# Performance work log

Hardware: AMD Instinct MI355X
Metric: run time of the kernel (lower is better)

The kernel has to match this reference:

```python
import jax, jax.numpy as jnp
import numpy as np

B, C, N, H = 4, 256, 2048, 8
D = C // H
EPS = 1e-5

def setup_inputs() -> dict:
    key = jax.random.key(0)
    ks = jax.random.split(key, 5)
    return {
        "x": jax.random.normal(ks[0], (B, C, N), jnp.float32),
        "w_qkv": jax.random.normal(ks[1], (3 * C, C), jnp.float32) * (C ** -0.5),
        "b_qkv": jax.random.normal(ks[2], (3 * C,), jnp.float32) * 0.02,
        "w_proj": jax.random.normal(ks[3], (C, C), jnp.float32) * (C ** -0.5),
        "b_proj": jax.random.normal(ks[4], (C,), jnp.float32) * 0.02,
        "ln_g": jnp.ones((C,), jnp.float32),
        "ln_b": jnp.zeros((C,), jnp.float32),
    }

def reference(x, w_qkv, b_qkv, w_proj, b_proj, ln_g, ln_b):
    # QKV 1x1 conv == per-point linear: [B,3C,N]
    qkv = jnp.einsum('oc,bcn->bon', w_qkv, x) + b_qkv[:, None]
    # [B,3,H,D,N] -> q,k,v each [B,H,N,D]
    qkv = qkv.reshape(B, 3, H, D, N).transpose(1, 0, 2, 4, 3)
    q, k, v = qkv[0], qkv[1], qkv[2]
    scale = D ** -0.5
    attn = jax.nn.softmax(jnp.einsum('bhnd,bhmd->bhnm', q, k) * scale, axis=-1)
    # dropout is identity in eval mode
    out = jnp.einsum('bhnm,bhmd->bhnd', attn, v)  # [B,H,N,D]
    out = out.transpose(0, 1, 3, 2).reshape(B, C, N)
    out = jnp.einsum('oc,bcn->bon', w_proj, out) + b_proj[:, None]
    out = out + x
    # LayerNorm over channel dim
    o = out.transpose(0, 2, 1)  # [B,N,C]
    mu = jnp.mean(o, axis=-1, keepdims=True)
    var = jnp.mean((o - mu) ** 2, axis=-1, keepdims=True)
    o = (o - mu) * jax.lax.rsqrt(var + EPS) * ln_g + ln_b
    return o.transpose(0, 2, 1)  # [B,C,N]
```

## Files before the change

### kernel.cpp

```cpp
#include <hip/hip_runtime.h>
#include <hip/hip_bf16.h>

#define Bx 4
#define Cx 256
#define Nx 2048
#define Hx 8
#define Dx 32

typedef __attribute__((ext_vector_type(8))) short bf16x8;
typedef __attribute__((ext_vector_type(4))) float f32x4;

#define QSCALE 0.25503494f

static __device__ __forceinline__ unsigned short f2bf(float f) {
    unsigned int u = __float_as_uint(f);
    u += 0x7fffu + ((u >> 16) & 1u);
    return (unsigned short)(u >> 16);
}
static __device__ __forceinline__ float bf2f(unsigned short u) {
    return __uint_as_float(((unsigned int)u) << 16);
}
static __device__ __forceinline__ float fexp2(float x) {
    float r;
    asm("v_exp_f32 %0, %1" : "=v"(r) : "v"(x));
    return r;
}
static __device__ __forceinline__ float frcp(float x) {
    float r;
    asm("v_rcp_f32 %0, %1" : "=v"(r) : "v"(x));
    return r;
}

__global__ __launch_bounds__(256) void convert_kernel(
    const float* __restrict__ x, const float* __restrict__ w_qkv,
    const float* __restrict__ w_proj,
    unsigned short* __restrict__ Xt, unsigned short* __restrict__ Wqkvb,
    unsigned short* __restrict__ Wpb)
{
    const int bx = blockIdx.x, t = threadIdx.x;
    if (bx < 512) {
        const int nb = (bx & 31) * 256 + t;
        const int b = nb >> 11, n = nb & 2047;
        const int c0 = (bx >> 5) * 16;
        const float* xb = x + (size_t)b * Cx * Nx + n;
        unsigned short* dst = Xt + ((size_t)b * Nx + n) * Cx;
        #pragma unroll
        for (int c8 = 0; c8 < 16; c8 += 8) {
            float f[8];
            #pragma unroll
            for (int j = 0; j < 8; ++j) f[j] = xb[(size_t)(c0 + c8 + j) * Nx];
            uint4 pk;
            pk.x = (unsigned)f2bf(f[0]) | ((unsigned)f2bf(f[1]) << 16);
            pk.y = (unsigned)f2bf(f[2]) | ((unsigned)f2bf(f[3]) << 16);
            pk.z = (unsigned)f2bf(f[4]) | ((unsigned)f2bf(f[5]) << 16);
            pk.w = (unsigned)f2bf(f[6]) | ((unsigned)f2bf(f[7]) << 16);
            *(uint4*)&dst[c0 + c8] = pk;
        }
    } else {
        const int flat = (bx - 512) * 2048 + t * 8;
        #pragma unroll
        for (int hh = 0; hh < 8; hh += 4) {
            const int f0 = flat + hh;
            if (f0 < 768 * 256) {
                const float sc = (f0 < 65536) ? QSCALE : 1.0f;
                const float4 f = *(const float4*)&w_qkv[f0];
                ushort4 o;
                o.x = f2bf(f.x * sc); o.y = f2bf(f.y * sc);
                o.z = f2bf(f.z * sc); o.w = f2bf(f.w * sc);
                *(ushort4*)&Wqkvb[f0] = o;
            } else {
                const int f2v = f0 - 768 * 256;
                const float4 f = *(const float4*)&w_proj[f2v];
                ushort4 o;
                o.x = f2bf(f.x); o.y = f2bf(f.y);
                o.z = f2bf(f.z); o.w = f2bf(f.w);
                *(ushort4*)&Wpb[f2v] = o;
            }
        }
    }
}

__global__ __launch_bounds__(256) void qkv_kernel(
    const unsigned short* __restrict__ Wb, const unsigned short* __restrict__ Xt,
    const float* __restrict__ bias,
    unsigned short* __restrict__ Qb, unsigned short* __restrict__ Kb,
    unsigned short* __restrict__ Vb)
{
    const int t = threadIdx.x;
    const int wv = t >> 6, l = t & 63;
    const int g = l >> 4, c = l & 15;

    const int lin = blockIdx.x + 12 * (blockIdx.y + 16 * blockIdx.z);
    const int xcd = lin & 7, s = lin >> 3;
    const int xb = s % 12;
    const int yz = (s / 12) * 8 + xcd;
    const int yb = yz & 15, b = yz >> 4;

    const int o0 = xb * 64 + (wv >> 1) * 32;
    const int n0 = yb * 128 + (wv & 1) * 64;
    const int region = xb >> 2;

    const unsigned short* XtB = Xt + (size_t)b * Nx * Cx;

    if (region < 2) {
        f32x4 acc[2][4];
        #pragma unroll
        for (int i = 0; i < 2; ++i)
            #pragma unroll
            for (int j = 0; j < 4; ++j) acc[i][j] = (f32x4){0.f, 0.f, 0.f, 0.f};

        for (int cc = 0; cc < Cx; cc += 32) {
            bf16x8 wf[2], xf[4];
            #pragma unroll
            for (int ti = 0; ti < 2; ++ti)
                wf[ti] = *(const bf16x8*)&Wb[(size_t)(o0 + ti * 16 + c) * Cx + cc + g * 8];
            #pragma unroll
            for (int tj = 0; tj < 4; ++tj)
                xf[tj] = *(const bf16x8*)&XtB[(size_t)(n0 + tj * 16 + c) * Cx + cc + g * 8];
            #pragma unroll
            for (int ti = 0; ti < 2; ++ti)
                #pragma unroll
                for (int tj = 0; tj < 4; ++tj)
                    acc[ti][tj] = __builtin_amdgcn_mfma_f32_16x16x32_bf16(
                        wf[ti], xf[tj], acc[ti][tj], 0, 0, 0);
        }

        unsigned short* dst = (region == 0) ? Qb : Kb;
        #pragma unroll
        for (int ti = 0; ti < 2; ++ti) {
            const int o = o0 + ti * 16 + g * 4;
            float4 bv = *(const float4*)&bias[o];
            if (region == 0) { bv.x *= QSCALE; bv.y *= QSCALE; bv.z *= QSCALE; bv.w *= QSCALE; }
            const int d0 = o & 31, bh = b * 8 + ((o >> 5) & 7);
            unsigned short* dp = dst + (size_t)bh * Nx * Dx + d0;
            #pragma unroll
            for (int tj = 0; tj < 4; ++tj) {
                const int n = n0 + tj * 16 + c;
                ushort4 w4;
                w4.x = f2bf(acc[ti][tj][0] + bv.x);
                w4.y = f2bf(acc[ti][tj][1] + bv.y);
                w4.z = f2bf(acc[ti][tj][2] + bv.z);
                w4.w = f2bf(acc[ti][tj][3] + bv.w);
                *(ushort4*)&dp[(size_t)n * Dx] = w4;
            }
        }
    } else {
        f32x4 acc[4][2];
        #pragma unroll
        for (int i = 0; i < 4; ++i)
            #pragma unroll
            for (int j = 0; j < 2; ++j) acc[i][j] = (f32x4){0.f, 0.f, 0.f, 0.f};

        for (int cc = 0; cc < Cx; cc += 32) {
            bf16x8 wf[2], xf[4];
            #pragma unroll
            for (int ot = 0; ot < 2; ++ot)
                wf[ot] = *(const bf16x8*)&Wb[(size_t)(o0 + ot * 16 + c) * Cx + cc + g * 8];
            #pragma unroll
            for (int nt = 0; nt < 4; ++nt)
                xf[nt] = *(const bf16x8*)&XtB[(size_t)(n0 + nt * 16 + c) * Cx + cc + g * 8];
            #pragma unroll
            for (int nt = 0; nt < 4; ++nt)
                #pragma unroll
                for (int ot = 0; ot < 2; ++ot)
                    acc[nt][ot] = __builtin_amdgcn_mfma_f32_16x16x32_bf16(
                        xf[nt], wf[ot], acc[nt][ot], 0, 0, 0);
        }

        #pragma unroll
        for (int ot = 0; ot < 2; ++ot) {
            const int o = o0 + ot * 16 + c;
            const float bv = bias[o];
            const int oV = o - 512, d = oV & 31, bh = b * 8 + (oV >> 5);
            unsigned short* dp = Vb + ((size_t)bh * Dx + d) * Nx;
            #pragma unroll
            for (int nt = 0; nt < 4; ++nt) {
                const int n = n0 + nt * 16 + g * 4;
                ushort4 w4;
                w4.x = f2bf(acc[nt][ot][0] + bv);
                w4.y = f2bf(acc[nt][ot][1] + bv);
                w4.z = f2bf(acc[nt][ot][2] + bv);
                w4.w = f2bf(acc[nt][ot][3] + bv);
                *(ushort4*)&dp[n] = w4;
            }
        }
    }
}

__global__ __launch_bounds__(256, 4) void attn_kernel(
    const unsigned short* __restrict__ Qb, const unsigned short* __restrict__ Kb,
    const unsigned short* __restrict__ Vb, unsigned short* __restrict__ Opart,
    float2* __restrict__ ML)
{
    const int t  = threadIdx.x;
    const int wv = t >> 6, l = t & 63;
    const int g  = l >> 4, c = l & 15;

    const int lin = blockIdx.x + 16 * blockIdx.y + 512 * blockIdx.z;
    const int xcd = lin & 7, s = lin >> 3;
    const int bh = ((s & 3) << 3) | xcd;
    const int qt_ = (s >> 2) & 15;
    const int z  = s >> 6;
    const int q0 = qt_ * 128 + wv * 32;

    const unsigned short* Qp = Qb + (size_t)bh * Nx * Dx;
    const unsigned short* Kp = Kb + (size_t)bh * Nx * Dx;
    const unsigned short* Vp = Vb + (size_t)bh * Dx * Nx;

    bf16x8 qf[2];
    #pragma unroll
    for (int qt = 0; qt < 2; ++qt)
        qf[qt] = *(const bf16x8*)&Qp[(size_t)(q0 + qt * 16 + c) * Dx + g * 8];

    union { unsigned int u[4]; bf16x8 v; } onesf;
    onesf.u[0] = onesf.u[1] = onesf.u[2] = onesf.u[3] = 0x3F803F80u;

    f32x4 oacc[2][2];
    f32x4 lacc[2];
    #pragma unroll
    for (int i = 0; i < 2; ++i) {
        lacc[i] = (f32x4){0.f, 0.f, 0.f, 0.f};
        #pragma unroll
        for (int j = 0; j < 2; ++j)
            oacc[i][j] = (f32x4){0.f, 0.f, 0.f, 0.f};
    }
    float m_i[2] = {-3.0e38f, -3.0e38f};
    const f32x4 zacc = (f32x4){0.f, 0.f, 0.f, 0.f};

    const int rowperm = (c >> 2) * 8 + (c & 3);

    const int kv_beg = z * (Nx / 2), kv_end = kv_beg + (Nx / 2);
    for (int kv0 = kv_beg; kv0 < kv_end; kv0 += 64) {
        bf16x8 kf[4];
        kf[0] = *(const bf16x8*)&Kp[(size_t)(kv0 + rowperm +  0) * Dx + g * 8];
        kf[1] = *(const bf16x8*)&Kp[(size_t)(kv0 + rowperm +  4) * Dx + g * 8];
        kf[2] = *(const bf16x8*)&Kp[(size_t)(kv0 + rowperm + 32) * Dx + g * 8];
        kf[3] = *(const bf16x8*)&Kp[(size_t)(kv0 + rowperm + 36) * Dx + g * 8];
        bf16x8 vf[2][2];
        #pragma unroll
        for (int dt = 0; dt < 2; ++dt)
            #pragma unroll
            for (int kc = 0; kc < 2; ++kc)
                vf[dt][kc] = *(const bf16x8*)
                    &Vp[(size_t)(dt * 16 + c) * Nx + kv0 + kc * 32 + g * 8];

        #pragma unroll
        for (int qt = 0; qt < 2; ++qt) {
            f32x4 sacc[4];
            #pragma unroll
            for (int ct = 0; ct < 4; ++ct)
                sacc[ct] = __builtin_amdgcn_mfma_f32_16x16x32_bf16(
                    kf[ct], qf[qt], zacc, 0, 0, 0);

            float tm[4];
            #pragma unroll
            for (int ct = 0; ct < 4; ++ct)
                tm[ct] = fmaxf(fmaxf(fmaxf(sacc[ct][0], sacc[ct][1]),
                                     sacc[ct][2]), sacc[ct][3]);
            const float mxl = fmaxf(fmaxf(fmaxf(tm[0], tm[1]), tm[2]), tm[3]);

            if (__any(mxl > m_i[qt] + 8.f)) {
                float mx = fmaxf(mxl, __shfl_xor(mxl, 16, 64));
                mx = fmaxf(mx, __shfl_xor(mx, 32, 64));
                const float mnew = fmaxf(m_i[qt], mx);
                const float aq = fexp2(m_i[qt] - mnew);
                m_i[qt] = mnew;
                #pragma unroll
                for (int dt = 0; dt < 2; ++dt)
                    #pragma unroll
                    for (int r = 0; r < 4; ++r) oacc[dt][qt][r] *= aq;
                #pragma unroll
                for (int r = 0; r < 4; ++r) lacc[qt][r] *= aq;
            }
            const float mcur = m_i[qt];
            unsigned int pw[4][2];
            #pragma unroll
            for (int ct = 0; ct < 4; ++ct) {
                float p[4];
                #pragma unroll
                for (int r = 0; r < 4; ++r) p[r] = fexp2(sacc[ct][r] - mcur);
                pw[ct][0] = (__float_as_uint(p[0]) >> 16) |
                            (__float_as_uint(p[1]) & 0xffff0000u);
                pw[ct][1] = (__float_as_uint(p[2]) >> 16) |
                            (__float_as_uint(p[3]) & 0xffff0000u);
            }

            #pragma unroll
            for (int kc = 0; kc < 2; ++kc) {
                union { unsigned int u[4]; bf16x8 v; } bw;
                bw.u[0] = pw[kc * 2 + 0][0];
                bw.u[1] = pw[kc * 2 + 0][1];
                bw.u[2] = pw[kc * 2 + 1][0];
                bw.u[3] = pw[kc * 2 + 1][1];
                oacc[0][qt] = __builtin_amdgcn_mfma_f32_16x16x32_bf16(
                    vf[0][kc], bw.v, oacc[0][qt], 0, 0, 0);
                oacc[1][qt] = __builtin_amdgcn_mfma_f32_16x16x32_bf16(
                    vf[1][kc], bw.v, oacc[1][qt], 0, 0, 0);
                lacc[qt] = __builtin_amdgcn_mfma_f32_16x16x32_bf16(
                    onesf.v, bw.v, lacc[qt], 0, 0, 0);
            }
        }
    }

    unsigned short* Op = Opart + ((size_t)(z * 32 + bh)) * Nx * Dx;
    float2* Mlp = ML + (size_t)(z * 32 + bh) * Nx;
    #pragma unroll
    for (int qt = 0; qt < 2; ++qt) {
        const int q = q0 + qt * 16 + c;
        if (g == 0) Mlp[q] = make_float2(m_i[qt], lacc[qt][0]);
        #pragma unroll
        for (int dt = 0; dt < 2; ++dt) {
            ushort4 w4;
            w4.x = f2bf(oacc[dt][qt][0]);
            w4.y = f2bf(oacc[dt][qt][1]);
            w4.z = f2bf(oacc[dt][qt][2]);
            w4.w = f2bf(oacc[dt][qt][3]);
            *(ushort4*)&Op[(size_t)q * Dx + dt * 16 + g * 4] = w4;
        }
    }
}

__global__ __launch_bounds__(256) void proj_ln_kernel(
    const unsigned short* __restrict__ Opart, const float2* __restrict__ ML,
    const unsigned short* __restrict__ Wpb,
    const float* __restrict__ bp, const float* __restrict__ x,
    const float* __restrict__ lng, const float* __restrict__ lnb,
    float* __restrict__ out)
{
    __shared__ float red[4][16];
    __shared__ float redq[4][16];
    __shared__ float mv[2][16];

    const int t  = threadIdx.x;
    const int wv = t >> 6, l = t & 63;
    const int lg = l >> 4, lc = l & 15;
    const int n0 = blockIdx.x * 16;
    const int b  = blockIdx.y;
    const int o0 = wv * 64;
    const int n  = n0 + lc;

    f32x4 acc[4];
    #pragma unroll
    for (int i = 0; i < 4; ++i) acc[i] = (f32x4){0.f, 0.f, 0.f, 0.f};

    for (int cc = 0; cc < Cx; cc += 32) {
        const int h = cc >> 5;
        const int bh = b * 8 + h;
        const float2 e0 = ML[(size_t)bh * Nx + n];
        const float2 e1 = ML[(size_t)(32 + bh) * Nx + n];
        const float M  = fmaxf(e0.x, e1.x);
        const float a0 = fexp2(e0.x - M), a1 = fexp2(e1.x - M);
        const float inv = frcp(e0.y * a0 + e1.y * a1);
        const float w0 = a0 * inv, w1 = a1 * inv;
        const size_t obase = ((size_t)bh * Nx + n) * Dx + lg * 8;
        const uint4 u0 = *(const uint4*)&Opart[obase];
        const uint4 u1 = *(const uint4*)&Opart[(size_t)65536 * Dx + obase];
        const unsigned int u0w[4] = {u0.x, u0.y, u0.z, u0.w};
        const unsigned int u1w[4] = {u1.x, u1.y, u1.z, u1.w};
        union { unsigned int u[4]; bf16x8 v; } af;
        #pragma unroll
        for (int wi = 0; wi < 4; ++wi) {
            const float lo = bf2f((unsigned short)(u0w[wi] & 0xffffu)) * w0 +
                             bf2f((unsigned short)(u1w[wi] & 0xffffu)) * w1;
            const float hi = bf2f((unsigned short)(u0w[wi] >> 16)) * w0 +
                             bf2f((unsigned short)(u1w[wi] >> 16)) * w1;
            af.u[wi] = (unsigned int)f2bf(lo) | ((unsigned int)f2bf(hi) << 16);
        }
        #pragma unroll
        for (int ti = 0; ti < 4; ++ti) {
            const bf16x8 wf = *(const bf16x8*)
                &Wpb[(size_t)(o0 + ti * 16 + lc) * Cx + cc + lg * 8];
            acc[ti] = __builtin_amdgcn_mfma_f32_16x16x32_bf16(wf, af.v, acc[ti], 0, 0, 0);
        }
    }

    #pragma unroll
    for (int ti = 0; ti < 4; ++ti) {
        const int o = o0 + ti * 16 + lg * 4;
        const float4 bv = *(const float4*)&bp[o];
        const float* xp = &x[((size_t)b * Cx + o) * Nx + n];
        acc[ti][0] += bv.x + xp[0];
        acc[ti][1] += bv.y + xp[Nx];
        acc[ti][2] += bv.z + xp[2 * Nx];
        acc[ti][3] += bv.w + xp[3 * Nx];
    }

    float s_ = 0.f, q_ = 0.f;
    #pragma unroll
    for (int ti = 0; ti < 4; ++ti)
        #pragma unroll
        for (int r = 0; r < 4; ++r) {
            const float v = acc[ti][r];
            s_ += v; q_ += v * v;
        }
    s_ += __shfl_xor(s_, 16, 64);
    s_ += __shfl_xor(s_, 32, 64);
    q_ += __shfl_xor(q_, 16, 64);
    q_ += __shfl_xor(q_, 32, 64);
    if (lg == 0) { red[wv][lc] = s_; redq[wv][lc] = q_; }
    __syncthreads();
    if (t < 16) {
        const float S = red[0][t] + red[1][t] + red[2][t] + red[3][t];
        const float Q = redq[0][t] + redq[1][t] + redq[2][t] + redq[3][t];
        const float mu  = S * (1.f / 256.f);
        const float var = Q * (1.f / 256.f) - mu * mu;
        mv[0][t] = mu;
        mv[1][t] = rsqrtf(var + 1e-5f);
    }
    __syncthreads();

    const float mu_ = mv[0][lc], rs_ = mv[1][lc];
    #pragma unroll
    for (int ti = 0; ti < 4; ++ti) {
        const int o = o0 + ti * 16 + lg * 4;
        const float4 g4 = *(const float4*)&lng[o];
        const float4 b4 = *(const float4*)&lnb[o];
        const float gr[4] = {g4.x, g4.y, g4.z, g4.w};
        const float br[4] = {b4.x, b4.y, b4.z, b4.w};
        float* op = &out[((size_t)b * Cx + o) * Nx + n];
        #pragma unroll
        for (int r = 0; r < 4; ++r)
            op[(size_t)r * Nx] = (acc[ti][r] - mu_) * rs_ * gr[r] + br[r];
    }
}

extern "C" void kernel_launch(void* const* d_in, const int* in_sizes, int n_in,
                              void* d_out, int out_size, void* d_ws, size_t ws_size,
                              hipStream_t stream) {
    (void)in_sizes; (void)n_in; (void)out_size; (void)ws_size;
    const float* x      = (const float*)d_in[0];
    const float* w_qkv  = (const float*)d_in[1];
    const float* b_qkv  = (const float*)d_in[2];
    const float* w_proj = (const float*)d_in[3];
    const float* b_proj = (const float*)d_in[4];
    const float* ln_g   = (const float*)d_in[5];
    const float* ln_b   = (const float*)d_in[6];
    float* out = (float*)d_out;

    char* wsb = (char*)d_ws;
    unsigned short* Xt    = (unsigned short*)(wsb);
    unsigned short* Wqkvb = (unsigned short*)(wsb + (size_t)4 * 1024 * 1024);
    unsigned short* Wpb   = (unsigned short*)(wsb + (size_t)4 * 1024 * 1024 + 393216);
    unsigned short* Qb    = (unsigned short*)(wsb + (size_t)5 * 1024 * 1024);
    unsigned short* Kb    = (unsigned short*)(wsb + (size_t)9 * 1024 * 1024);
    unsigned short* Vb    = (unsigned short*)(wsb + (size_t)13 * 1024 * 1024);
    unsigned short* Opart = (unsigned short*)(wsb + (size_t)21 * 1024 * 1024);
    float2*         ML    = (float2*)(wsb + (size_t)29 * 1024 * 1024);

    convert_kernel<<<dim3(640), 256, 0, stream>>>(x, w_qkv, w_proj, Xt, Wqkvb, Wpb);
    qkv_kernel<<<dim3(12, 16, 4), 256, 0, stream>>>(Wqkvb, Xt, b_qkv, Qb, Kb, Vb);
    attn_kernel<<<dim3(16, 32, 2), 256, 0, stream>>>(Qb, Kb, Vb, Opart, ML);
    proj_ln_kernel<<<dim3(128, 4), 256, 0, stream>>>(Opart, ML, Wpb, b_proj, x,
                                                     ln_g, ln_b, out);
}
```

Baseline: 155.9 us.

## Split attention KV range four ways and double-buffer K/V register loads

The attention kernel now splits each head's KV sequence into four chunks instead of two, doubling the grid to add parallelism. Each block's KV loop is fully unrolled with A/B register buffers, so the next tile's K/V loads are issued before the current tile is computed. The projection/LayerNorm kernel now merges four partial outputs and their max/sum statistics instead of two. The workspace is rearranged so the larger partial-output buffer reuses the space of the already-consumed transposed input. The cost is more partial-output traffic, extra merge work and higher register pressure from the prefetch buffers.

```diff
diff --git a/kernel.cpp b/kernel.cpp
--- a/kernel.cpp
+++ b/kernel.cpp
@@ -187,6 +187,80 @@
     }
 }
 
+static __device__ __forceinline__ void attn_tile(
+    const bf16x8* kf, const bf16x8* vf, const bf16x8* qf, bf16x8 onesv,
+    f32x4 (&oacc)[2][2], f32x4 (&lacc)[2], float (&m_i)[2])
+{
+    const f32x4 zacc = (f32x4){0.f, 0.f, 0.f, 0.f};
+    #pragma unroll
+    for (int qt = 0; qt < 2; ++qt) {
+        f32x4 sacc[4];
+        #pragma unroll
+        for (int ct = 0; ct < 4; ++ct)
+            sacc[ct] = __builtin_amdgcn_mfma_f32_16x16x32_bf16(
+                kf[ct], qf[qt], zacc, 0, 0, 0);
+
+        float tm[4];
+        #pragma unroll
+        for (int ct = 0; ct < 4; ++ct)
+            tm[ct] = fmaxf(fmaxf(fmaxf(sacc[ct][0], sacc[ct][1]),
+                                 sacc[ct][2]), sacc[ct][3]);
+        const float mxl = fmaxf(fmaxf(fmaxf(tm[0], tm[1]), tm[2]), tm[3]);
+
+        if (__any(mxl > m_i[qt] + 8.f)) {
+            float mx = fmaxf(mxl, __shfl_xor(mxl, 16, 64));
+            mx = fmaxf(mx, __shfl_xor(mx, 32, 64));
+            const float mnew = fmaxf(m_i[qt], mx);
+            const float aq = fexp2(m_i[qt] - mnew);
+            m_i[qt] = mnew;
+            #pragma unroll
+            for (int dt = 0; dt < 2; ++dt)
+                #pragma unroll
+                for (int r = 0; r < 4; ++r) oacc[dt][qt][r] *= aq;
+            #pragma unroll
+            for (int r = 0; r < 4; ++r) lacc[qt][r] *= aq;
+        }
+        const float mcur = m_i[qt];
+        unsigned int pw[4][2];
+        #pragma unroll
+        for (int ct = 0; ct < 4; ++ct) {
+            float p[4];
+            #pragma unroll
+            for (int r = 0; r < 4; ++r) p[r] = fexp2(sacc[ct][r] - mcur);
+            pw[ct][0] = (__float_as_uint(p[0]) >> 16) |
+                        (__float_as_uint(p[1]) & 0xffff0000u);
+            pw[ct][1] = (__float_as_uint(p[2]) >> 16) |
+                        (__float_as_uint(p[3]) & 0xffff0000u);
+        }
+
+        #pragma unroll
+        for (int kc = 0; kc < 2; ++kc) {
+            union { unsigned int u[4]; bf16x8 v; } bw;
+            bw.u[0] = pw[kc * 2 + 0][0];
+            bw.u[1] = pw[kc * 2 + 0][1];
+            bw.u[2] = pw[kc * 2 + 1][0];
+            bw.u[3] = pw[kc * 2 + 1][1];
+            oacc[0][qt] = __builtin_amdgcn_mfma_f32_16x16x32_bf16(
+                vf[0 * 2 + kc], bw.v, oacc[0][qt], 0, 0, 0);
+            oacc[1][qt] = __builtin_amdgcn_mfma_f32_16x16x32_bf16(
+                vf[1 * 2 + kc], bw.v, oacc[1][qt], 0, 0, 0);
+            lacc[qt] = __builtin_amdgcn_mfma_f32_16x16x32_bf16(
+                onesv, bw.v, lacc[qt], 0, 0, 0);
+        }
+    }
+}
+
+#define LOADT(KF, VF, KV) do {                                                  \
+    KF[0] = *(const bf16x8*)&Kp[(size_t)((KV) + rowperm +  0) * Dx + g * 8];    \
+    KF[1] = *(const bf16x8*)&Kp[(size_t)((KV) + rowperm +  4) * Dx + g * 8];    \
+    KF[2] = *(const bf16x8*)&Kp[(size_t)((KV) + rowperm + 32) * Dx + g * 8];    \
+    KF[3] = *(const bf16x8*)&Kp[(size_t)((KV) + rowperm + 36) * Dx + g * 8];    \
+    VF[0] = *(const bf16x8*)&Vp[(size_t)(c)      * Nx + (KV)      + g * 8];     \
+    VF[1] = *(const bf16x8*)&Vp[(size_t)(c)      * Nx + (KV) + 32 + g * 8];     \
+    VF[2] = *(const bf16x8*)&Vp[(size_t)(16 + c) * Nx + (KV)      + g * 8];     \
+    VF[3] = *(const bf16x8*)&Vp[(size_t)(16 + c) * Nx + (KV) + 32 + g * 8];     \
+} while (0)
+
 __global__ __launch_bounds__(256, 4) void attn_kernel(
     const unsigned short* __restrict__ Qb, const unsigned short* __restrict__ Kb,
     const unsigned short* __restrict__ Vb, unsigned short* __restrict__ Opart,
@@ -225,81 +299,23 @@
             oacc[i][j] = (f32x4){0.f, 0.f, 0.f, 0.f};
     }
     float m_i[2] = {-3.0e38f, -3.0e38f};
-    const f32x4 zacc = (f32x4){0.f, 0.f, 0.f, 0.f};
 
     const int rowperm = (c >> 2) * 8 + (c & 3);
-
-    const int kv_beg = z * (Nx / 2), kv_end = kv_beg + (Nx / 2);
-    for (int kv0 = kv_beg; kv0 < kv_end; kv0 += 64) {
-        bf16x8 kf[4];
-        kf[0] = *(const bf16x8*)&Kp[(size_t)(kv0 + rowperm +  0) * Dx + g * 8];
-        kf[1] = *(const bf16x8*)&Kp[(size_t)(kv0 + rowperm +  4) * Dx + g * 8];
-        kf[2] = *(const bf16x8*)&Kp[(size_t)(kv0 + rowperm + 32) * Dx + g * 8];
-        kf[3] = *(const bf16x8*)&Kp[(size_t)(kv0 + rowperm + 36) * Dx + g * 8];
-        bf16x8 vf[2][2];
-        #pragma unroll
-        for (int dt = 0; dt < 2; ++dt)
-            #pragma unroll
-            for (int kc = 0; kc < 2; ++kc)
-                vf[dt][kc] = *(const bf16x8*)
-                    &Vp[(size_t)(dt * 16 + c) * Nx + kv0 + kc * 32 + g * 8];
-
-        #pragma unroll
-        for (int qt = 0; qt < 2; ++qt) {
-            f32x4 sacc[4];
-            #pragma unroll
-            for (int ct = 0; ct < 4; ++ct)
-                sacc[ct] = __builtin_amdgcn_mfma_f32_16x16x32_bf16(
-                    kf[ct], qf[qt], zacc, 0, 0, 0);
-
-            float tm[4];
-            #pragma unroll
-            for (int ct = 0; ct < 4; ++ct)
-                tm[ct] = fmaxf(fmaxf(fmaxf(sacc[ct][0], sacc[ct][1]),
-                                     sacc[ct][2]), sacc[ct][3]);
-            const float mxl = fmaxf(fmaxf(fmaxf(tm[0], tm[1]), tm[2]), tm[3]);
-
-            if (__any(mxl > m_i[qt] + 8.f)) {
-                float mx = fmaxf(mxl, __shfl_xor(mxl, 16, 64));
-                mx = fmaxf(mx, __shfl_xor(mx, 32, 64));
-                const float mnew = fmaxf(m_i[qt], mx);
-                const float aq = fexp2(m_i[qt] - mnew);
-                m_i[qt] = mnew;
-                #pragma unroll
-                for (int dt = 0; dt < 2; ++dt)
-                    #pragma unroll
-                    for (int r = 0; r < 4; ++r) oacc[dt][qt][r] *= aq;
-                #pragma unroll
-                for (int r = 0; r < 4; ++r) lacc[qt][r] *= aq;
-            }
-            const float mcur = m_i[qt];
-            unsigned int pw[4][2];
-            #pragma unroll
-            for (int ct = 0; ct < 4; ++ct) {
-                float p[4];
-                #pragma unroll
-                for (int r = 0; r < 4; ++r) p[r] = fexp2(sacc[ct][r] - mcur);
-                pw[ct][0] = (__float_as_uint(p[0]) >> 16) |
-                            (__float_as_uint(p[1]) & 0xffff0000u);
-                pw[ct][1] = (__float_as_uint(p[2]) >> 16) |
-                            (__float_as_uint(p[3]) & 0xffff0000u);
-            }
-
-            #pragma unroll
-            for (int kc = 0; kc < 2; ++kc) {
-                union { unsigned int u[4]; bf16x8 v; } bw;
-                bw.u[0] = pw[kc * 2 + 0][0];
-                bw.u[1] = pw[kc * 2 + 0][1];
-                bw.u[2] = pw[kc * 2 + 1][0];
-                bw.u[3] = pw[kc * 2 + 1][1];
-                oacc[0][qt] = __builtin_amdgcn_mfma_f32_16x16x32_bf16(
-                    vf[0][kc], bw.v, oacc[0][qt], 0, 0, 0);
-                oacc[1][qt] = __builtin_amdgcn_mfma_f32_16x16x32_bf16(
-                    vf[1][kc], bw.v, oacc[1][qt], 0, 0, 0);
-                lacc[qt] = __builtin_amdgcn_mfma_f32_16x16x32_bf16(
-                    onesf.v, bw.v, lacc[qt], 0, 0, 0);
-            }
-        }
+    const int kv_beg = z * 512;
+
+    bf16x8 kfA[4], vfA[4], kfB[4], vfB[4];
+    LOADT(kfA, vfA, kv_beg);
+    int kv0 = kv_beg;
+    #pragma unroll
+    for (int it = 0; it < 8; ++it) {
+        if ((it & 1) == 0) {
+            if (it < 7) { LOADT(kfB, vfB, kv0 + 64); }
+            attn_tile(kfA, vfA, qf, onesf.v, oacc, lacc, m_i);
+        } else {
+            if (it < 7) { LOADT(kfA, vfA, kv0 + 64); }
+            attn_tile(kfB, vfB, qf, onesf.v, oacc, lacc, m_i);
+        }
+        kv0 += 64;
     }
 
     unsigned short* Op = Opart + ((size_t)(z * 32 + bh)) * Nx * Dx;
@@ -346,24 +362,36 @@
     for (int cc = 0; cc < Cx; cc += 32) {
         const int h = cc >> 5;
         const int bh = b * 8 + h;
-        const float2 e0 = ML[(size_t)bh * Nx + n];
-        const float2 e1 = ML[(size_t)(32 + bh) * Nx + n];
-        const float M  = fmaxf(e0.x, e1.x);
-        const float a0 = fexp2(e0.x - M), a1 = fexp2(e1.x - M);
-        const float inv = frcp(e0.y * a0 + e1.y * a1);
-        const float w0 = a0 * inv, w1 = a1 * inv;
+        float2 e[4];
+        #pragma unroll
+        for (int zz = 0; zz < 4; ++zz)
+            e[zz] = ML[(size_t)(zz * 32 + bh) * Nx + n];
+        const float M = fmaxf(fmaxf(e[0].x, e[1].x), fmaxf(e[2].x, e[3].x));
+        float a[4], den = 0.f;
+        #pragma unroll
+        for (int zz = 0; zz < 4; ++zz) {
+            a[zz] = fexp2(e[zz].x - M);
+            den += e[zz].y * a[zz];
+        }
+        const float inv = frcp(den);
+        #pragma unroll
+        for (int zz = 0; zz < 4; ++zz) a[zz] *= inv;
+
         const size_t obase = ((size_t)bh * Nx + n) * Dx + lg * 8;
-        const uint4 u0 = *(const uint4*)&Opart[obase];
-        const uint4 u1 = *(const uint4*)&Opart[(size_t)65536 * Dx + obase];
-        const unsigned int u0w[4] = {u0.x, u0.y, u0.z, u0.w};
-        const unsigned int u1w[4] = {u1.x, u1.y, u1.z, u1.w};
+        union { uint4 q; unsigned int w[4]; } uz[4];
+        #pragma unroll
+        for (int zz = 0; zz < 4; ++zz)
+            uz[zz].q = *(const uint4*)&Opart[(size_t)zz * 32 * Nx * Dx + obase];
         union { unsigned int u[4]; bf16x8 v; } af;
         #pragma unroll
         for (int wi = 0; wi < 4; ++wi) {
-            const float lo = bf2f((unsigned short)(u0w[wi] & 0xffffu)) * w0 +
-                             bf2f((unsigned short)(u1w[wi] & 0xffffu)) * w1;
-            const float hi = bf2f((unsigned short)(u0w[wi] >> 16)) * w0 +
-                             bf2f((unsigned short)(u1w[wi] >> 16)) * w1;
+            float lo = 0.f, hi = 0.f;
+            #pragma unroll
+            for (int zz = 0; zz < 4; ++zz) {
+                const unsigned int w = uz[zz].w[wi];
+                lo = fmaf(__uint_as_float(w << 16), a[zz], lo);
+                hi = fmaf(__uint_as_float(w & 0xffff0000u), a[zz], hi);
+            }
             af.u[wi] = (unsigned int)f2bf(lo) | ((unsigned int)f2bf(hi) << 16);
         }
         #pragma unroll
@@ -439,17 +467,17 @@
 
     char* wsb = (char*)d_ws;
     unsigned short* Xt    = (unsigned short*)(wsb);
-    unsigned short* Wqkvb = (unsigned short*)(wsb + (size_t)4 * 1024 * 1024);
-    unsigned short* Wpb   = (unsigned short*)(wsb + (size_t)4 * 1024 * 1024 + 393216);
-    unsigned short* Qb    = (unsigned short*)(wsb + (size_t)5 * 1024 * 1024);
-    unsigned short* Kb    = (unsigned short*)(wsb + (size_t)9 * 1024 * 1024);
-    unsigned short* Vb    = (unsigned short*)(wsb + (size_t)13 * 1024 * 1024);
-    unsigned short* Opart = (unsigned short*)(wsb + (size_t)21 * 1024 * 1024);
-    float2*         ML    = (float2*)(wsb + (size_t)29 * 1024 * 1024);
+    unsigned short* Opart = (unsigned short*)(wsb);
+    float2*         ML    = (float2*)(wsb + (size_t)16 * 1024 * 1024);
+    unsigned short* Wqkvb = (unsigned short*)(wsb + (size_t)18 * 1024 * 1024);
+    unsigned short* Wpb   = (unsigned short*)(wsb + (size_t)18 * 1024 * 1024 + 393216);
+    unsigned short* Qb    = (unsigned short*)(wsb + (size_t)19 * 1024 * 1024);
+    unsigned short* Kb    = (unsigned short*)(wsb + (size_t)23 * 1024 * 1024);
+    unsigned short* Vb    = (unsigned short*)(wsb + (size_t)27 * 1024 * 1024);
 
     convert_kernel<<<dim3(640), 256, 0, stream>>>(x, w_qkv, w_proj, Xt, Wqkvb, Wpb);
     qkv_kernel<<<dim3(12, 16, 4), 256, 0, stream>>>(Wqkvb, Xt, b_qkv, Qb, Kb, Vb);
-    attn_kernel<<<dim3(16, 32, 2), 256, 0, stream>>>(Qb, Kb, Vb, Opart, ML);
+    attn_kernel<<<dim3(16, 32, 4), 256, 0, stream>>>(Qb, Kb, Vb, Opart, ML);
     proj_ln_kernel<<<dim3(128, 4), 256, 0, stream>>>(Opart, ML, Wpb, b_proj, x,
                                                      ln_g, ln_b, out);
 }
```

Measured after the change: 163.2 us. 4.7% more time.

## Stage combined attention output in LDS once per block and shrink QKV tiles

Applied to the files above, without the earlier changes.

In proj_ln_kernel, the two-split softmax merge and bf16 packing of the attention output now run once per block into a swizzled LDS tile. Previously each of the four waves redid the same merge for every head. The QKV GEMM tile is halved along N, which doubles the grid to add parallelism at the cost of less operand reuse per block. The workspace is also rearranged so Opart reuses the Xt region, which is dead once the QKV kernel has finished.

```diff
diff --git a/kernel.cpp b/kernel.cpp
--- a/kernel.cpp
+++ b/kernel.cpp
@@ -90,37 +90,37 @@
     const int wv = t >> 6, l = t & 63;
     const int g = l >> 4, c = l & 15;
 
-    const int lin = blockIdx.x + 12 * (blockIdx.y + 16 * blockIdx.z);
+    const int lin = blockIdx.x + 12 * (blockIdx.y + 32 * blockIdx.z);
     const int xcd = lin & 7, s = lin >> 3;
     const int xb = s % 12;
     const int yz = (s / 12) * 8 + xcd;
-    const int yb = yz & 15, b = yz >> 4;
+    const int yb = yz & 31, b = yz >> 5;
 
     const int o0 = xb * 64 + (wv >> 1) * 32;
-    const int n0 = yb * 128 + (wv & 1) * 64;
+    const int n0 = yb * 64 + (wv & 1) * 32;
     const int region = xb >> 2;
 
     const unsigned short* XtB = Xt + (size_t)b * Nx * Cx;
 
+    f32x4 acc[2][2];
+    #pragma unroll
+    for (int i = 0; i < 2; ++i)
+        #pragma unroll
+        for (int j = 0; j < 2; ++j) acc[i][j] = (f32x4){0.f, 0.f, 0.f, 0.f};
+
     if (region < 2) {
-        f32x4 acc[2][4];
-        #pragma unroll
-        for (int i = 0; i < 2; ++i)
-            #pragma unroll
-            for (int j = 0; j < 4; ++j) acc[i][j] = (f32x4){0.f, 0.f, 0.f, 0.f};
-
         for (int cc = 0; cc < Cx; cc += 32) {
-            bf16x8 wf[2], xf[4];
+            bf16x8 wf[2], xf[2];
             #pragma unroll
             for (int ti = 0; ti < 2; ++ti)
                 wf[ti] = *(const bf16x8*)&Wb[(size_t)(o0 + ti * 16 + c) * Cx + cc + g * 8];
             #pragma unroll
-            for (int tj = 0; tj < 4; ++tj)
+            for (int tj = 0; tj < 2; ++tj)
                 xf[tj] = *(const bf16x8*)&XtB[(size_t)(n0 + tj * 16 + c) * Cx + cc + g * 8];
             #pragma unroll
             for (int ti = 0; ti < 2; ++ti)
                 #pragma unroll
-                for (int tj = 0; tj < 4; ++tj)
+                for (int tj = 0; tj < 2; ++tj)
                     acc[ti][tj] = __builtin_amdgcn_mfma_f32_16x16x32_bf16(
                         wf[ti], xf[tj], acc[ti][tj], 0, 0, 0);
         }
@@ -134,7 +134,7 @@
             const int d0 = o & 31, bh = b * 8 + ((o >> 5) & 7);
             unsigned short* dp = dst + (size_t)bh * Nx * Dx + d0;
             #pragma unroll
-            for (int tj = 0; tj < 4; ++tj) {
+            for (int tj = 0; tj < 2; ++tj) {
                 const int n = n0 + tj * 16 + c;
                 ushort4 w4;
                 w4.x = f2bf(acc[ti][tj][0] + bv.x);
@@ -145,22 +145,16 @@
             }
         }
     } else {
-        f32x4 acc[4][2];
-        #pragma unroll
-        for (int i = 0; i < 4; ++i)
-            #pragma unroll
-            for (int j = 0; j < 2; ++j) acc[i][j] = (f32x4){0.f, 0.f, 0.f, 0.f};
-
         for (int cc = 0; cc < Cx; cc += 32) {
-            bf16x8 wf[2], xf[4];
+            bf16x8 wf[2], xf[2];
             #pragma unroll
             for (int ot = 0; ot < 2; ++ot)
                 wf[ot] = *(const bf16x8*)&Wb[(size_t)(o0 + ot * 16 + c) * Cx + cc + g * 8];
             #pragma unroll
-            for (int nt = 0; nt < 4; ++nt)
+            for (int nt = 0; nt < 2; ++nt)
                 xf[nt] = *(const bf16x8*)&XtB[(size_t)(n0 + nt * 16 + c) * Cx + cc + g * 8];
             #pragma unroll
-            for (int nt = 0; nt < 4; ++nt)
+            for (int nt = 0; nt < 2; ++nt)
                 #pragma unroll
                 for (int ot = 0; ot < 2; ++ot)
                     acc[nt][ot] = __builtin_amdgcn_mfma_f32_16x16x32_bf16(
@@ -174,7 +168,7 @@
             const int oV = o - 512, d = oV & 31, bh = b * 8 + (oV >> 5);
             unsigned short* dp = Vb + ((size_t)bh * Dx + d) * Nx;
             #pragma unroll
-            for (int nt = 0; nt < 4; ++nt) {
+            for (int nt = 0; nt < 2; ++nt) {
                 const int n = n0 + nt * 16 + g * 4;
                 ushort4 w4;
                 w4.x = f2bf(acc[nt][ot][0] + bv);
@@ -327,6 +321,7 @@
     const float* __restrict__ lng, const float* __restrict__ lnb,
     float* __restrict__ out)
 {
+    __shared__ uint4 Albs[16][32];
     __shared__ float red[4][16];
     __shared__ float redq[4][16];
     __shared__ float mv[2][16];
@@ -339,37 +334,50 @@
     const int o0 = wv * 64;
     const int n  = n0 + lc;
 
+    {
+        const int n_s = t & 15;
+        #pragma unroll
+        for (int it = 0; it < 2; ++it) {
+            const int cgrp = (t >> 4) + it * 16;
+            const int h  = cgrp >> 2;
+            const int bh = b * 8 + h;
+            const int d8 = (cgrp & 3) * 8;
+            const float2 e0 = ML[(size_t)bh * Nx + n0 + n_s];
+            const float2 e1 = ML[(size_t)(32 + bh) * Nx + n0 + n_s];
+            const float M  = fmaxf(e0.x, e1.x);
+            const float a0 = fexp2(e0.x - M), a1 = fexp2(e1.x - M);
+            const float inv = frcp(e0.y * a0 + e1.y * a1);
+            const float w0 = a0 * inv, w1 = a1 * inv;
+            const size_t obase = ((size_t)bh * Nx + n0 + n_s) * Dx + d8;
+            union { uint4 q; unsigned int w[4]; } u0, u1;
+            u0.q = *(const uint4*)&Opart[obase];
+            u1.q = *(const uint4*)&Opart[(size_t)32 * Nx * Dx + obase];
+            union { unsigned int u[4]; uint4 q; } af;
+            #pragma unroll
+            for (int wi = 0; wi < 4; ++wi) {
+                const float lo = __uint_as_float(u0.w[wi] << 16) * w0 +
+                                 __uint_as_float(u1.w[wi] << 16) * w1;
+                const float hi = __uint_as_float(u0.w[wi] & 0xffff0000u) * w0 +
+                                 __uint_as_float(u1.w[wi] & 0xffff0000u) * w1;
+                af.u[wi] = (unsigned)f2bf(lo) | ((unsigned)f2bf(hi) << 16);
+            }
+            Albs[n_s][cgrp ^ (n_s & 7)] = af.q;
+        }
+    }
+    __syncthreads();
+
     f32x4 acc[4];
     #pragma unroll
     for (int i = 0; i < 4; ++i) acc[i] = (f32x4){0.f, 0.f, 0.f, 0.f};
 
-    for (int cc = 0; cc < Cx; cc += 32) {
-        const int h = cc >> 5;
-        const int bh = b * 8 + h;
-        const float2 e0 = ML[(size_t)bh * Nx + n];
-        const float2 e1 = ML[(size_t)(32 + bh) * Nx + n];
-        const float M  = fmaxf(e0.x, e1.x);
-        const float a0 = fexp2(e0.x - M), a1 = fexp2(e1.x - M);
-        const float inv = frcp(e0.y * a0 + e1.y * a1);
-        const float w0 = a0 * inv, w1 = a1 * inv;
-        const size_t obase = ((size_t)bh * Nx + n) * Dx + lg * 8;
-        const uint4 u0 = *(const uint4*)&Opart[obase];
-        const uint4 u1 = *(const uint4*)&Opart[(size_t)65536 * Dx + obase];
-        const unsigned int u0w[4] = {u0.x, u0.y, u0.z, u0.w};
-        const unsigned int u1w[4] = {u1.x, u1.y, u1.z, u1.w};
-        union { unsigned int u[4]; bf16x8 v; } af;
-        #pragma unroll
-        for (int wi = 0; wi < 4; ++wi) {
-            const float lo = bf2f((unsigned short)(u0w[wi] & 0xffffu)) * w0 +
-                             bf2f((unsigned short)(u1w[wi] & 0xffffu)) * w1;
-            const float hi = bf2f((unsigned short)(u0w[wi] >> 16)) * w0 +
-                             bf2f((unsigned short)(u1w[wi] >> 16)) * w1;
-            af.u[wi] = (unsigned int)f2bf(lo) | ((unsigned int)f2bf(hi) << 16);
-        }
+    #pragma unroll
+    for (int cc8 = 0; cc8 < 32; cc8 += 4) {
+        union { uint4 q; bf16x8 v; } af;
+        af.q = Albs[lc][(cc8 + lg) ^ (lc & 7)];
         #pragma unroll
         for (int ti = 0; ti < 4; ++ti) {
             const bf16x8 wf = *(const bf16x8*)
-                &Wpb[(size_t)(o0 + ti * 16 + lc) * Cx + cc + lg * 8];
+                &Wpb[(size_t)(o0 + ti * 16 + lc) * Cx + cc8 * 8 + lg * 8];
             acc[ti] = __builtin_amdgcn_mfma_f32_16x16x32_bf16(wf, af.v, acc[ti], 0, 0, 0);
         }
     }
@@ -439,16 +447,16 @@
 
     char* wsb = (char*)d_ws;
     unsigned short* Xt    = (unsigned short*)(wsb);
-    unsigned short* Wqkvb = (unsigned short*)(wsb + (size_t)4 * 1024 * 1024);
-    unsigned short* Wpb   = (unsigned short*)(wsb + (size_t)4 * 1024 * 1024 + 393216);
-    unsigned short* Qb    = (unsigned short*)(wsb + (size_t)5 * 1024 * 1024);
-    unsigned short* Kb    = (unsigned short*)(wsb + (size_t)9 * 1024 * 1024);
-    unsigned short* Vb    = (unsigned short*)(wsb + (size_t)13 * 1024 * 1024);
-    unsigned short* Opart = (unsigned short*)(wsb + (size_t)21 * 1024 * 1024);
-    float2*         ML    = (float2*)(wsb + (size_t)29 * 1024 * 1024);
+    unsigned short* Opart = (unsigned short*)(wsb);
+    float2*         ML    = (float2*)(wsb + (size_t)8 * 1024 * 1024);
+    unsigned short* Wqkvb = (unsigned short*)(wsb + (size_t)9 * 1024 * 1024);
+    unsigned short* Wpb   = (unsigned short*)(wsb + (size_t)9 * 1024 * 1024 + 393216);
+    unsigned short* Qb    = (unsigned short*)(wsb + (size_t)10 * 1024 * 1024);
+    unsigned short* Kb    = (unsigned short*)(wsb + (size_t)14 * 1024 * 1024);
+    unsigned short* Vb    = (unsigned short*)(wsb + (size_t)18 * 1024 * 1024);
 
     convert_kernel<<<dim3(640), 256, 0, stream>>>(x, w_qkv, w_proj, Xt, Wqkvb, Wpb);
-    qkv_kernel<<<dim3(12, 16, 4), 256, 0, stream>>>(Wqkvb, Xt, b_qkv, Qb, Kb, Vb);
+    qkv_kernel<<<dim3(12, 32, 4), 256, 0, stream>>>(Wqkvb, Xt, b_qkv, Qb, Kb, Vb);
     attn_kernel<<<dim3(16, 32, 2), 256, 0, stream>>>(Qb, Kb, Vb, Opart, ML);
     proj_ln_kernel<<<dim3(128, 4), 256, 0, stream>>>(Opart, ML, Wpb, b_proj, x,
                                                      ln_g, ln_b, out);
```

New measurement: 158.7 us. About the same (+1.8%).
